# Kernel tuning notes

Measured on AMD Instinct MI355X. Metric: run time of the kernel, lower is better.

Reference implementation:

```python
import jax, jax.numpy as jnp
import numpy as np

N_NODES = 50000
N_EDGES = 800000
D_IN = 16


def gcn_conv(x, edge_index, W, b, n_nodes):
    """PyG GCNConv: x' = D^{-1/2} (A + I) D^{-1/2} X W + b (add_self_loops=True)."""
    h = x @ W  # [N, d_out] - transform before propagate (small d => cheaper)
    src = jnp.concatenate([edge_index[0], jnp.arange(n_nodes)])  # add self-loops
    dst = jnp.concatenate([edge_index[1], jnp.arange(n_nodes)])
    deg = jax.ops.segment_sum(jnp.ones_like(dst, dtype=h.dtype), dst,
                              num_segments=n_nodes)  # in-degree incl. self-loop
    deg_inv_sqrt = jnp.where(deg > 0, jax.lax.rsqrt(deg), 0.0)
    norm = deg_inv_sqrt[src] * deg_inv_sqrt[dst]  # [E+N]
    msg = h[src] * norm[:, None]                  # gather + scale
    out = jax.ops.segment_sum(msg, dst, num_segments=n_nodes)  # scatter-add
    return out + b


def setup_inputs() -> dict:
    key = jax.random.key(0)
    ks = jax.random.split(key, 16)
    d = D_IN
    x = jax.random.normal(ks[0], (N_NODES, d), dtype=jnp.float32)
    edge_index = jax.random.randint(ks[1], (2, N_EDGES), 0, N_NODES, dtype=jnp.int64)

    def glorot(k, fan_in, fan_out):
        s = (6.0 / (fan_in + fan_out)) ** 0.5
        return jax.random.uniform(k, (fan_in, fan_out), jnp.float32, -s, s)

    return {
        "x": x,
        "edge_index": edge_index,
        "W1": glorot(ks[2], d, 2 * d),      "b1": jnp.zeros((2 * d,), jnp.float32),
        "W2": glorot(ks[3], 2 * d, 4 * d),  "b2": jnp.zeros((4 * d,), jnp.float32),
        "W3": glorot(ks[4], 4 * d, 8 * d),  "b3": jnp.zeros((8 * d,), jnp.float32),
        "Wl1": glorot(ks[5], 8 * d, 4 * d), "bl1": jnp.zeros((4 * d,), jnp.float32),
        "Wl2": glorot(ks[6], 4 * d, 2 * d), "bl2": jnp.zeros((2 * d,), jnp.float32),
        "Wl3": glorot(ks[7], 2 * d, d),     "bl3": jnp.zeros((d,), jnp.float32),
    }


def reference(x, edge_index, W1, b1, W2, b2, W3, b3, Wl1, bl1, Wl2, bl2, Wl3, bl3):
    n = x.shape[0]
    # note: original applies relu twice per conv; relu is idempotent
    out = jax.nn.relu(gcn_conv(x, edge_index, W1, b1, n))
    out = jax.nn.relu(gcn_conv(out, edge_index, W2, b2, n))
    out = jax.nn.relu(gcn_conv(out, edge_index, W3, b3, n))
    out = jax.nn.relu(out @ Wl1 + bl1)
    out = jax.nn.relu(out @ Wl2 + bl2)
    out = jax.nn.relu(out @ Wl3 + bl3)
    return out
```

## Files before the change

kernel.cpp:

```cpp
#include <hip/hip_runtime.h>

#define TPB 256
#define TE  2048
#define MAXB 6144

typedef _Float16 half_t;
typedef _Float16 half4 __attribute__((ext_vector_type(4)));
typedef _Float16 half8 __attribute__((ext_vector_type(8)));
typedef float float8v __attribute__((ext_vector_type(8)));

static inline int cdiv(int a, int b) { return (a + b - 1) / b; }


__global__ void k_zero_int(int* p, int n) {
    int i = blockIdx.x * blockDim.x + threadIdx.x;
    if (i < n) p[i] = 0;
}

__global__ void k_bhist(const int* __restrict__ dst, int* __restrict__ gcnt,
                        int e, int nb) {
    __shared__ int lc[256];
    for (int t = threadIdx.x; t < nb; t += TPB) lc[t] = 0;
    __syncthreads();
    for (int i = blockIdx.x * TPB + threadIdx.x; i < e; i += gridDim.x * TPB)
        atomicAdd(&lc[dst[i] >> 8], 1);
    __syncthreads();
    for (int t = threadIdx.x; t < nb; t += TPB) {
        int v = lc[t];
        if (v) atomicAdd(&gcnt[t], v);
    }
}

__global__ void k_bscan(const int* __restrict__ gcnt, int* __restrict__ bstart,
                        int* __restrict__ bcur, int nb, int e) {
    __shared__ int s[256];
    int t = threadIdx.x;
    int v = (t < nb) ? gcnt[t] : 0;
    s[t] = v;
    __syncthreads();
    for (int d = 1; d < 256; d <<= 1) {
        int x = (t >= d) ? s[t - d] : 0;
        __syncthreads();
        s[t] += x;
        __syncthreads();
    }
    if (t < nb) { int ex = s[t] - v; bstart[t] = ex; bcur[t] = ex; }
    if (t == 0) bstart[nb] = e;
}

__global__ void __launch_bounds__(TPB)
k_binscatter(const int* __restrict__ src, const int* __restrict__ dst,
             int* __restrict__ bcur, unsigned int* __restrict__ gbuf,
             int e, int nb) {
    __shared__ int lcnt[256], loffs[256], lcur[256], gres[256];
    __shared__ int ss[256];
    __shared__ unsigned int ldata[TE];
    const int base = blockIdx.x * TE;
    const int cnt = min(TE, e - base);
    for (int t = threadIdx.x; t < nb; t += TPB) lcnt[t] = 0;
    __syncthreads();

    unsigned int myv[TE / TPB];
    int myb[TE / TPB];
#pragma unroll
    for (int k = 0; k < TE / TPB; ++k) {
        int j = threadIdx.x + k * TPB;
        if (j < cnt) {
            int d = dst[base + j], s = src[base + j];
            int b = d >> 8;
            myv[k] = ((unsigned)b << 24) | ((unsigned)(d & 255) << 16) | (unsigned)s;
            myb[k] = b;
            atomicAdd(&lcnt[b], 1);
        } else myb[k] = -1;
    }
    __syncthreads();
    {
        int t = threadIdx.x;
        int v = (t < nb) ? lcnt[t] : 0;
        ss[t] = v;
        __syncthreads();
        for (int d = 1; d < 256; d <<= 1) {
            int x = (t >= d) ? ss[t - d] : 0;
            __syncthreads();
            ss[t] += x;
            __syncthreads();
        }
        if (t < nb) { loffs[t] = ss[t] - v; lcur[t] = ss[t] - v; }
    }
    __syncthreads();
    for (int t = threadIdx.x; t < nb; t += TPB)
        if (lcnt[t]) gres[t] = atomicAdd(&bcur[t], lcnt[t]);
#pragma unroll
    for (int k = 0; k < TE / TPB; ++k) {
        if (myb[k] >= 0) {
            int p = atomicAdd(&lcur[myb[k]], 1);
            ldata[p] = myv[k];
        }
    }
    __syncthreads();
    for (int j = threadIdx.x; j < cnt; j += TPB) {
        unsigned int v = ldata[j];
        int b = v >> 24;
        gbuf[gres[b] + (j - loffs[b])] = v & 0xFFFFFFu;
    }
}

__global__ void __launch_bounds__(TPB)
k_csr(const unsigned int* __restrict__ gbuf, const int* __restrict__ bstart,
      int* __restrict__ offs, float* __restrict__ dinv, int* __restrict__ ssrc,
      int n, int e) {
    __shared__ int cnt[256], loffs2[256], lcur2[256], ss[256];
    __shared__ int stage[MAXB];
    const int b = blockIdx.x;
    const int s0 = bstart[b], s1 = bstart[b + 1];
    const int m = s1 - s0;
    cnt[threadIdx.x] = 0;
    __syncthreads();
    for (int j = threadIdx.x; j < m; j += TPB)
        atomicAdd(&cnt[(gbuf[s0 + j] >> 16) & 255], 1);
    __syncthreads();
    {
        int t = threadIdx.x;
        int v = cnt[t];
        ss[t] = v;
        __syncthreads();
        for (int d = 1; d < 256; d <<= 1) {
            int x = (t >= d) ? ss[t - d] : 0;
            __syncthreads();
            ss[t] += x;
            __syncthreads();
        }
        loffs2[t] = ss[t] - v;
        lcur2[t] = ss[t] - v;
        int node = b * 256 + t;
        if (node < n) {
            offs[node] = s0 + loffs2[t];
            dinv[node] = rsqrtf((float)v + 1.0f);
        }
    }
    __syncthreads();
    for (int j = threadIdx.x; j < m; j += TPB) {
        unsigned int v = gbuf[s0 + j];
        int p = atomicAdd(&lcur2[(v >> 16) & 255], 1);
        stage[p] = (int)(v & 0xFFFFu);
    }
    __syncthreads();
    for (int j = threadIdx.x; j < m; j += TPB) ssrc[s0 + j] = stage[j];
    if (b == 0 && threadIdx.x == 0) offs[n] = e;
}


__global__ void k_scale(const float* __restrict__ x, const float* __restrict__ dinv,
                        half_t* __restrict__ G, int n) {
    int idx = blockIdx.x * blockDim.x + threadIdx.x;
    if (idx >= n * 2) return;
    float d = dinv[idx >> 1];
    float8v v = ((const float8v*)x)[idx];
    half8 h;
#pragma unroll
    for (int q = 0; q < 8; ++q) h[q] = (half_t)(v[q] * d);
    ((half8*)G)[idx] = h;
}

template<int DI, int DO, int R, bool SCALE, bool OUT_HALF, bool WHALF>
__global__ void __launch_bounds__(TPB, 4)
k_conv(const int* __restrict__ offs, const int* __restrict__ ssrc,
       const half_t* __restrict__ G, const float* __restrict__ dinv,
       const float* __restrict__ W, const float* __restrict__ b,
       void* __restrict__ outp, int n) {
    constexpr int CT = DO / 4;
    constexpr int RT = TPB / CT;
    constexpr int TM = RT * R;
    constexpr int K4 = DI / 4;
    constexpr int PX = K4 + 1;
    constexpr int C  = DI / 8;
    static_assert(TM * C == TPB, "gather/gemm tile mismatch");
    __shared__ float4 sW4[WHALF ? 1 : DI * CT];
    __shared__ half4  sWh[WHALF ? DI * CT : 1];
    __shared__ float4 sX4[TM * PX];
    const int tid = threadIdx.x;
    const int r0 = blockIdx.x * TM;

    const float4* Wg = (const float4*)W;
    for (int t = tid; t < DI * CT; t += TPB) {
        float4 w = Wg[t];
        if (WHALF) {
            half4 h;
            h.x = (half_t)w.x; h.y = (half_t)w.y;
            h.z = (half_t)w.z; h.w = (half_t)w.w;
            sWh[t] = h;
        } else {
            sW4[t] = w;
        }
    }

    {
        int gr = tid / C;
        int gc = tid - gr * C;
        int row = r0 + gr;
        float8v acc;
#pragma unroll
        for (int q = 0; q < 8; ++q) acc[q] = 0.f;
        if (row < n) {
            const half8* Grow = (const half8*)G;
            half8 hs = Grow[(size_t)row * C + gc];
#pragma unroll
            for (int q = 0; q < 8; ++q) acc[q] = (float)hs[q];
            int s0 = offs[row], s1 = offs[row + 1];
            int j = s0;
            for (; j + 3 < s1; j += 4) {
                int sa = ssrc[j], sb = ssrc[j + 1];
                int sc = ssrc[j + 2], sd = ssrc[j + 3];
                half8 ga = Grow[(size_t)sa * C + gc];
                half8 gb = Grow[(size_t)sb * C + gc];
                half8 gch = Grow[(size_t)sc * C + gc];
                half8 gd = Grow[(size_t)sd * C + gc];
#pragma unroll
                for (int q = 0; q < 8; ++q)
                    acc[q] += ((float)ga[q] + (float)gb[q]) + ((float)gch[q] + (float)gd[q]);
            }
            for (; j < s1; ++j) {
                half8 ga = Grow[(size_t)ssrc[j] * C + gc];
#pragma unroll
                for (int q = 0; q < 8; ++q) acc[q] += (float)ga[q];
            }
            float di = dinv[row];
#pragma unroll
            for (int q = 0; q < 8; ++q) acc[q] *= di;
        }
        sX4[gr * PX + 2 * gc]     = make_float4(acc[0], acc[1], acc[2], acc[3]);
        sX4[gr * PX + 2 * gc + 1] = make_float4(acc[4], acc[5], acc[6], acc[7]);
    }
    __syncthreads();

    const int c = tid & (CT - 1);
    const int rg = tid / CT;
    const int rbase = rg * R;
    float4 acc[R];
#pragma unroll
    for (int r = 0; r < R; ++r) acc[r] = make_float4(0.f, 0.f, 0.f, 0.f);

#pragma unroll 2
    for (int k4 = 0; k4 < K4; ++k4) {
        float4 xv[R];
#pragma unroll
        for (int r = 0; r < R; ++r) xv[r] = sX4[(rbase + r) * PX + k4];
#pragma unroll
        for (int kk = 0; kk < 4; ++kk) {
            float4 wv;
            if (WHALF) {
                half4 wh = sWh[(k4 * 4 + kk) * CT + c];
                wv = make_float4((float)wh.x, (float)wh.y, (float)wh.z, (float)wh.w);
            } else {
                wv = sW4[(k4 * 4 + kk) * CT + c];
            }
#pragma unroll
            for (int r = 0; r < R; ++r) {
                float xs = (kk == 0) ? xv[r].x : (kk == 1) ? xv[r].y
                         : (kk == 2) ? xv[r].z : xv[r].w;
                acc[r].x += xs * wv.x; acc[r].y += xs * wv.y;
                acc[r].z += xs * wv.z; acc[r].w += xs * wv.w;
            }
        }
    }

    float4 bc = ((const float4*)b)[c];
#pragma unroll
    for (int r = 0; r < R; ++r) {
        int row = r0 + rbase + r;
        if (row < n) {
            float4 o;
            o.x = fmaxf(acc[r].x + bc.x, 0.f);
            o.y = fmaxf(acc[r].y + bc.y, 0.f);
            o.z = fmaxf(acc[r].z + bc.z, 0.f);
            o.w = fmaxf(acc[r].w + bc.w, 0.f);
            if (SCALE) {
                float d = dinv[row];
                o.x *= d; o.y *= d; o.z *= d; o.w *= d;
            }
            if (OUT_HALF) {
                half4 h;
                h.x = (half_t)o.x; h.y = (half_t)o.y;
                h.z = (half_t)o.z; h.w = (half_t)o.w;
                ((half4*)outp)[(size_t)row * CT + c] = h;
            } else {
                ((float4*)outp)[(size_t)row * CT + c] = o;
            }
        }
    }
}

__global__ void __launch_bounds__(256, 2)
k_head(const half_t* __restrict__ X,
       const float* __restrict__ W1, const float* __restrict__ b1,
       const float* __restrict__ W2, const float* __restrict__ b2,
       const float* __restrict__ W3, const float* __restrict__ b3,
       float* __restrict__ out, int n) {
    __shared__ half_t hW1[128 * 64];
    __shared__ half_t hW2[64 * 32];
    __shared__ half_t hW3[32 * 16];
    __shared__ float h1[64 * 65];
    __shared__ float h2[64 * 33];
    const int tid = threadIdx.x;
    const int r0 = blockIdx.x * 64;

    for (int t = tid; t < 128 * 64; t += 256) hW1[t] = (half_t)W1[t];
    for (int t = tid; t < 64 * 32; t += 256) hW2[t] = (half_t)W2[t];
    for (int t = tid; t < 32 * 16; t += 256) hW3[t] = (half_t)W3[t];
    __syncthreads();

    {
        const int c4 = tid & 15;
        const int rowg = tid >> 4;
        const half8* Xr = (const half8*)X;
        float acc[4][4];
#pragma unroll
        for (int r = 0; r < 4; ++r)
#pragma unroll
            for (int j = 0; j < 4; ++j) acc[r][j] = 0.f;
        for (int k8 = 0; k8 < 16; ++k8) {
            half8 xh[4];
#pragma unroll
            for (int r = 0; r < 4; ++r) {
                int row = r0 + rowg * 4 + r;
                if (row < n) xh[r] = Xr[(size_t)row * 16 + k8];
                else { half8 z; for (int q = 0; q < 8; ++q) z[q] = (half_t)0.f; xh[r] = z; }
            }
#pragma unroll
            for (int q = 0; q < 8; ++q) {
                int k = k8 * 8 + q;
                half4 w = *(const half4*)&hW1[k * 64 + c4 * 4];
                float w0 = (float)w.x, w1 = (float)w.y, w2 = (float)w.z, w3 = (float)w.w;
#pragma unroll
                for (int r = 0; r < 4; ++r) {
                    float xs = (float)xh[r][q];
                    acc[r][0] += xs * w0; acc[r][1] += xs * w1;
                    acc[r][2] += xs * w2; acc[r][3] += xs * w3;
                }
            }
        }
        float4 bc = ((const float4*)b1)[c4];
#pragma unroll
        for (int r = 0; r < 4; ++r) {
            int rl = rowg * 4 + r;
            h1[rl * 65 + c4 * 4 + 0] = fmaxf(acc[r][0] + bc.x, 0.f);
            h1[rl * 65 + c4 * 4 + 1] = fmaxf(acc[r][1] + bc.y, 0.f);
            h1[rl * 65 + c4 * 4 + 2] = fmaxf(acc[r][2] + bc.z, 0.f);
            h1[rl * 65 + c4 * 4 + 3] = fmaxf(acc[r][3] + bc.w, 0.f);
        }
    }
    __syncthreads();

    {
        const int c4 = tid & 7;
        const int rowg = tid >> 3;
        float acc[2][4];
#pragma unroll
        for (int r = 0; r < 2; ++r)
#pragma unroll
            for (int j = 0; j < 4; ++j) acc[r][j] = 0.f;
#pragma unroll 4
        for (int k = 0; k < 64; ++k) {
            half4 w = *(const half4*)&hW2[k * 32 + c4 * 4];
            float w0 = (float)w.x, w1 = (float)w.y, w2 = (float)w.z, w3 = (float)w.w;
#pragma unroll
            for (int r = 0; r < 2; ++r) {
                float xs = h1[(rowg * 2 + r) * 65 + k];
                acc[r][0] += xs * w0; acc[r][1] += xs * w1;
                acc[r][2] += xs * w2; acc[r][3] += xs * w3;
            }
        }
        float4 bc = ((const float4*)b2)[c4];
#pragma unroll
        for (int r = 0; r < 2; ++r) {
            int rl = rowg * 2 + r;
            h2[rl * 33 + c4 * 4 + 0] = fmaxf(acc[r][0] + bc.x, 0.f);
            h2[rl * 33 + c4 * 4 + 1] = fmaxf(acc[r][1] + bc.y, 0.f);
            h2[rl * 33 + c4 * 4 + 2] = fmaxf(acc[r][2] + bc.z, 0.f);
            h2[rl * 33 + c4 * 4 + 3] = fmaxf(acc[r][3] + bc.w, 0.f);
        }
    }
    __syncthreads();

    {
        const int c4 = tid & 3;
        const int rl = tid >> 2;
        float a0 = 0.f, a1 = 0.f, a2 = 0.f, a3 = 0.f;
#pragma unroll 4
        for (int k = 0; k < 32; ++k) {
            half4 w = *(const half4*)&hW3[k * 16 + c4 * 4];
            float xs = h2[rl * 33 + k];
            a0 += xs * (float)w.x; a1 += xs * (float)w.y;
            a2 += xs * (float)w.z; a3 += xs * (float)w.w;
        }
        int row = r0 + rl;
        if (row < n) {
            float4 bc = ((const float4*)b3)[c4];
            float4 o;
            o.x = fmaxf(a0 + bc.x, 0.f);
            o.y = fmaxf(a1 + bc.y, 0.f);
            o.z = fmaxf(a2 + bc.z, 0.f);
            o.w = fmaxf(a3 + bc.w, 0.f);
            ((float4*)out)[(size_t)row * 4 + c4] = o;
        }
    }
}

extern "C" void kernel_launch(void* const* d_in, const int* in_sizes, int n_in,
                              void* d_out, int out_size, void* d_ws, size_t ws_size,
                              hipStream_t stream) {
    const float* x   = (const float*)d_in[0];
    const int*   ei  = (const int*)d_in[1];
    const float* W1  = (const float*)d_in[2];
    const float* bb1 = (const float*)d_in[3];
    const float* W2  = (const float*)d_in[4];
    const float* bb2 = (const float*)d_in[5];
    const float* W3  = (const float*)d_in[6];
    const float* bb3 = (const float*)d_in[7];
    const float* Wl1 = (const float*)d_in[8];
    const float* bl1 = (const float*)d_in[9];
    const float* Wl2 = (const float*)d_in[10];
    const float* bl2 = (const float*)d_in[11];
    const float* Wl3 = (const float*)d_in[12];
    const float* bl3 = (const float*)d_in[13];
    float* out = (float*)d_out;

    const int n = in_sizes[0] / 16;
    const int e = in_sizes[1] / 2;
    const int* src = ei;
    const int* dst = ei + e;
    const int nb = cdiv(n, 256);

    char* p = (char*)d_ws;
    auto alloc = [&](size_t bytes) {
        char* r = p;
        p += (bytes + 255) & ~(size_t)255;
        return r;
    };
    float*        dinv   = (float*)        alloc((size_t)n * 4);
    int*          offs   = (int*)          alloc((size_t)(n + 1) * 4);
    int*          gcnt   = (int*)          alloc(256 * 4);
    int*          bstart = (int*)          alloc(257 * 4);
    int*          bcur   = (int*)          alloc(256 * 4);
    unsigned int* gbuf   = (unsigned int*) alloc((size_t)e * 4);
    int*          ssrc   = (int*)          alloc((size_t)e * 4);
    half_t*       H1     = (half_t*)       alloc((size_t)n * 64 * 2);
    half_t*       H2     = (half_t*)       alloc((size_t)n * 32 * 2);
    half_t*       X3h    = (half_t*)       alloc((size_t)n * 128 * 2);

    k_zero_int<<<1, 256, 0, stream>>>(gcnt, nb);
    k_bhist<<<512, TPB, 0, stream>>>(dst, gcnt, e, nb);
    k_bscan<<<1, 256, 0, stream>>>(gcnt, bstart, bcur, nb, e);
    k_binscatter<<<cdiv(e, TE), TPB, 0, stream>>>(src, dst, bcur, gbuf, e, nb);
    k_csr<<<nb, TPB, 0, stream>>>(gbuf, bstart, offs, dinv, ssrc, n, e);

    k_scale<<<cdiv(n * 2, TPB), TPB, 0, stream>>>(x, dinv, H1, n);
    k_conv<16, 32, 4, true, true, false><<<cdiv(n, 128), TPB, 0, stream>>>(
        offs, ssrc, H1, dinv, W1, bb1, H2, n);
    k_conv<32, 64, 4, true, true, false><<<cdiv(n, 64), TPB, 0, stream>>>(
        offs, ssrc, H2, dinv, W2, bb2, H1, n);
    k_conv<64, 128, 4, false, true, true><<<cdiv(n, 32), TPB, 0, stream>>>(
        offs, ssrc, H1, dinv, W3, bb3, X3h, n);

    k_head<<<cdiv(n, 64), 256, 0, stream>>>(X3h, Wl1, bl1, Wl2, bl2, Wl3, bl3, out, n);
}
```

Before: 219.6 us.

## Fuse scan and scale into CSR build, shrink source indices, degree-sort conv rows

Removes the standalone bucket-scan kernel by recomputing the prefix scan redundantly in each binscatter and CSR block. The bcur2 cursors start at zero (zeroed alongside gcnt) and are added to the per-block scan result. The x scaling is folded into the CSR kernel, and source indices are stored as 16-bit values to halve index traffic. Each conv block sorts its rows by degree so lanes with similar edge counts run together, which adds a small rank computation and extra syncs per block. The 16-bit indices rely on node ids fitting in 16 bits (N=50000).

```diff
diff --git a/kernel.cpp b/kernel.cpp
--- a/kernel.cpp
+++ b/kernel.cpp
@@ -31,40 +31,37 @@
     }
 }
 
-__global__ void k_bscan(const int* __restrict__ gcnt, int* __restrict__ bstart,
-                        int* __restrict__ bcur, int nb, int e) {
-    __shared__ int s[256];
-    int t = threadIdx.x;
-    int v = (t < nb) ? gcnt[t] : 0;
-    s[t] = v;
-    __syncthreads();
-    for (int d = 1; d < 256; d <<= 1) {
-        int x = (t >= d) ? s[t - d] : 0;
-        __syncthreads();
-        s[t] += x;
-        __syncthreads();
-    }
-    if (t < nb) { int ex = s[t] - v; bstart[t] = ex; bcur[t] = ex; }
-    if (t == 0) bstart[nb] = e;
-}
-
 __global__ void __launch_bounds__(TPB)
 k_binscatter(const int* __restrict__ src, const int* __restrict__ dst,
-             int* __restrict__ bcur, unsigned int* __restrict__ gbuf,
-             int e, int nb) {
+             const int* __restrict__ gcnt, int* __restrict__ bcur2,
+             unsigned int* __restrict__ gbuf, int e, int nb) {
     __shared__ int lcnt[256], loffs[256], lcur[256], gres[256];
     __shared__ int ss[256];
     __shared__ unsigned int ldata[TE];
+    const int tid = threadIdx.x;
     const int base = blockIdx.x * TE;
     const int cnt = min(TE, e - base);
-    for (int t = threadIdx.x; t < nb; t += TPB) lcnt[t] = 0;
+
+    {
+        int v = (tid < nb) ? gcnt[tid] : 0;
+        ss[tid] = v;
+        __syncthreads();
+        for (int d = 1; d < 256; d <<= 1) {
+            int x2 = (tid >= d) ? ss[tid - d] : 0;
+            __syncthreads();
+            ss[tid] += x2;
+            __syncthreads();
+        }
+        gres[tid] = ss[tid] - v;
+        lcnt[tid] = 0;
+    }
     __syncthreads();
 
     unsigned int myv[TE / TPB];
     int myb[TE / TPB];
 #pragma unroll
     for (int k = 0; k < TE / TPB; ++k) {
-        int j = threadIdx.x + k * TPB;
+        int j = tid + k * TPB;
         if (j < cnt) {
             int d = dst[base + j], s = src[base + j];
             int b = d >> 8;
@@ -75,21 +72,19 @@
     }
     __syncthreads();
     {
-        int t = threadIdx.x;
-        int v = (t < nb) ? lcnt[t] : 0;
-        ss[t] = v;
+        int v = (tid < nb) ? lcnt[tid] : 0;
+        ss[tid] = v;
         __syncthreads();
         for (int d = 1; d < 256; d <<= 1) {
-            int x = (t >= d) ? ss[t - d] : 0;
-            __syncthreads();
-            ss[t] += x;
-            __syncthreads();
-        }
-        if (t < nb) { loffs[t] = ss[t] - v; lcur[t] = ss[t] - v; }
-    }
-    __syncthreads();
-    for (int t = threadIdx.x; t < nb; t += TPB)
-        if (lcnt[t]) gres[t] = atomicAdd(&bcur[t], lcnt[t]);
+            int x2 = (tid >= d) ? ss[tid - d] : 0;
+            __syncthreads();
+            ss[tid] += x2;
+            __syncthreads();
+        }
+        if (tid < nb) { loffs[tid] = ss[tid] - v; lcur[tid] = ss[tid] - v; }
+    }
+    __syncthreads();
+    if (tid < nb && lcnt[tid]) gres[tid] += atomicAdd(&bcur2[tid], lcnt[tid]);
 #pragma unroll
     for (int k = 0; k < TE / TPB; ++k) {
         if (myb[k] >= 0) {
@@ -98,7 +93,7 @@
         }
     }
     __syncthreads();
-    for (int j = threadIdx.x; j < cnt; j += TPB) {
+    for (int j = tid; j < cnt; j += TPB) {
         unsigned int v = ldata[j];
         int b = v >> 24;
         gbuf[gres[b] + (j - loffs[b])] = v & 0xFFFFFFu;
@@ -106,65 +101,84 @@
 }
 
 __global__ void __launch_bounds__(TPB)
-k_csr(const unsigned int* __restrict__ gbuf, const int* __restrict__ bstart,
-      int* __restrict__ offs, float* __restrict__ dinv, int* __restrict__ ssrc,
-      int n, int e) {
-    __shared__ int cnt[256], loffs2[256], lcur2[256], ss[256];
-    __shared__ int stage[MAXB];
+k_csr(const unsigned int* __restrict__ gbuf, const int* __restrict__ gcnt,
+      const float* __restrict__ x, int* __restrict__ offs,
+      float* __restrict__ dinv, unsigned short* __restrict__ ssrc,
+      half_t* __restrict__ G, int n, int e, int nb) {
+    __shared__ int ss[256], cnt[256], loffs2[256], lcur2[256];
+    __shared__ float sdinv[256];
+    __shared__ unsigned short stage[MAXB];
     const int b = blockIdx.x;
-    const int s0 = bstart[b], s1 = bstart[b + 1];
+    const int t = threadIdx.x;
+
+    {
+        int v = (t < nb) ? gcnt[t] : 0;
+        ss[t] = v;
+        __syncthreads();
+        for (int d = 1; d < 256; d <<= 1) {
+            int x2 = (t >= d) ? ss[t - d] : 0;
+            __syncthreads();
+            ss[t] += x2;
+            __syncthreads();
+        }
+    }
+    const int s0 = (b > 0) ? ss[b - 1] : 0;
+    const int s1 = ss[b];
     const int m = s1 - s0;
-    cnt[threadIdx.x] = 0;
-    __syncthreads();
-    for (int j = threadIdx.x; j < m; j += TPB)
+    __syncthreads();
+    cnt[t] = 0;
+    __syncthreads();
+    for (int j = t; j < m; j += TPB)
         atomicAdd(&cnt[(gbuf[s0 + j] >> 16) & 255], 1);
     __syncthreads();
     {
-        int t = threadIdx.x;
         int v = cnt[t];
         ss[t] = v;
         __syncthreads();
         for (int d = 1; d < 256; d <<= 1) {
-            int x = (t >= d) ? ss[t - d] : 0;
-            __syncthreads();
-            ss[t] += x;
+            int x2 = (t >= d) ? ss[t - d] : 0;
+            __syncthreads();
+            ss[t] += x2;
             __syncthreads();
         }
         loffs2[t] = ss[t] - v;
         lcur2[t] = ss[t] - v;
+        float di = rsqrtf((float)v + 1.0f);
+        sdinv[t] = di;
         int node = b * 256 + t;
         if (node < n) {
             offs[node] = s0 + loffs2[t];
-            dinv[node] = rsqrtf((float)v + 1.0f);
-        }
-    }
-    __syncthreads();
-    for (int j = threadIdx.x; j < m; j += TPB) {
+            dinv[node] = di;
+        }
+    }
+    __syncthreads();
+    for (int j = t; j < m; j += TPB) {
         unsigned int v = gbuf[s0 + j];
         int p = atomicAdd(&lcur2[(v >> 16) & 255], 1);
-        stage[p] = (int)(v & 0xFFFFu);
-    }
-    __syncthreads();
-    for (int j = threadIdx.x; j < m; j += TPB) ssrc[s0 + j] = stage[j];
-    if (b == 0 && threadIdx.x == 0) offs[n] = e;
-}
-
-
-__global__ void k_scale(const float* __restrict__ x, const float* __restrict__ dinv,
-                        half_t* __restrict__ G, int n) {
-    int idx = blockIdx.x * blockDim.x + threadIdx.x;
-    if (idx >= n * 2) return;
-    float d = dinv[idx >> 1];
-    float8v v = ((const float8v*)x)[idx];
-    half8 h;
-#pragma unroll
-    for (int q = 0; q < 8; ++q) h[q] = (half_t)(v[q] * d);
-    ((half8*)G)[idx] = h;
+        stage[p] = (unsigned short)(v & 0xFFFFu);
+    }
+    __syncthreads();
+    for (int j = t; j < m; j += TPB) ssrc[s0 + j] = stage[j];
+    if (b == 0 && t == 0) offs[n] = e;
+
+    const int base = b * 256;
+    const int cn = min(256, n - base);
+    const float4* X4 = (const float4*)x;
+    half4* G4 = (half4*)G;
+    for (int j = t; j < cn * 4; j += TPB) {
+        int nl = j >> 2, k4 = j & 3;
+        float4 v = X4[(size_t)(base + nl) * 4 + k4];
+        float d = sdinv[nl];
+        half4 h;
+        h.x = (half_t)(v.x * d); h.y = (half_t)(v.y * d);
+        h.z = (half_t)(v.z * d); h.w = (half_t)(v.w * d);
+        G4[(size_t)(base + nl) * 4 + k4] = h;
+    }
 }
 
 template<int DI, int DO, int R, bool SCALE, bool OUT_HALF, bool WHALF>
 __global__ void __launch_bounds__(TPB, 4)
-k_conv(const int* __restrict__ offs, const int* __restrict__ ssrc,
+k_conv(const int* __restrict__ offs, const unsigned short* __restrict__ ssrc,
        const half_t* __restrict__ G, const float* __restrict__ dinv,
        const float* __restrict__ W, const float* __restrict__ b,
        void* __restrict__ outp, int n) {
@@ -178,6 +192,8 @@
     __shared__ float4 sW4[WHALF ? 1 : DI * CT];
     __shared__ half4  sWh[WHALF ? DI * CT : 1];
     __shared__ float4 sX4[TM * PX];
+    __shared__ int soffs[TM + 1];
+    __shared__ unsigned char perm[TM];
     const int tid = threadIdx.x;
     const int r0 = blockIdx.x * TM;
 
@@ -193,11 +209,24 @@
             sW4[t] = w;
         }
     }
-
-    {
-        int gr = tid / C;
-        int gc = tid - gr * C;
-        int row = r0 + gr;
+    if (tid <= TM) soffs[tid] = offs[min(r0 + tid, n)];
+    __syncthreads();
+    if (tid < TM) {
+        int d = soffs[tid + 1] - soffs[tid];
+        int rank = 0;
+        for (int j = 0; j < TM; ++j) {
+            int dj = soffs[j + 1] - soffs[j];
+            rank += (dj > d) || (dj == d && j < tid);
+        }
+        perm[rank] = (unsigned char)tid;
+    }
+    __syncthreads();
+
+    {
+        int slot = tid / C;
+        int gc = tid - slot * C;
+        int lrow = perm[slot];
+        int row = r0 + lrow;
         float8v acc;
 #pragma unroll
         for (int q = 0; q < 8; ++q) acc[q] = 0.f;
@@ -206,7 +235,7 @@
             half8 hs = Grow[(size_t)row * C + gc];
 #pragma unroll
             for (int q = 0; q < 8; ++q) acc[q] = (float)hs[q];
-            int s0 = offs[row], s1 = offs[row + 1];
+            int s0 = soffs[lrow], s1 = soffs[lrow + 1];
             int j = s0;
             for (; j + 3 < s1; j += 4) {
                 int sa = ssrc[j], sb = ssrc[j + 1];
@@ -228,8 +257,8 @@
 #pragma unroll
             for (int q = 0; q < 8; ++q) acc[q] *= di;
         }
-        sX4[gr * PX + 2 * gc]     = make_float4(acc[0], acc[1], acc[2], acc[3]);
-        sX4[gr * PX + 2 * gc + 1] = make_float4(acc[4], acc[5], acc[6], acc[7]);
+        sX4[lrow * PX + 2 * gc]     = make_float4(acc[0], acc[1], acc[2], acc[3]);
+        sX4[lrow * PX + 2 * gc + 1] = make_float4(acc[4], acc[5], acc[6], acc[7]);
     }
     __syncthreads();
 
@@ -437,24 +466,21 @@
         p += (bytes + 255) & ~(size_t)255;
         return r;
     };
-    float*        dinv   = (float*)        alloc((size_t)n * 4);
-    int*          offs   = (int*)          alloc((size_t)(n + 1) * 4);
-    int*          gcnt   = (int*)          alloc(256 * 4);
-    int*          bstart = (int*)          alloc(257 * 4);
-    int*          bcur   = (int*)          alloc(256 * 4);
-    unsigned int* gbuf   = (unsigned int*) alloc((size_t)e * 4);
-    int*          ssrc   = (int*)          alloc((size_t)e * 4);
-    half_t*       H1     = (half_t*)       alloc((size_t)n * 64 * 2);
-    half_t*       H2     = (half_t*)       alloc((size_t)n * 32 * 2);
-    half_t*       X3h    = (half_t*)       alloc((size_t)n * 128 * 2);
-
-    k_zero_int<<<1, 256, 0, stream>>>(gcnt, nb);
+    float*          dinv   = (float*)         alloc((size_t)n * 4);
+    int*            offs   = (int*)           alloc((size_t)(n + 1) * 4);
+    int*            gcnt   = (int*)           alloc(256 * 4);
+    int*            bcur2  = (int*)           alloc(256 * 4);
+    unsigned int*   gbuf   = (unsigned int*)  alloc((size_t)e * 4);
+    unsigned short* ssrc   = (unsigned short*)alloc((size_t)e * 2);
+    half_t*         H1     = (half_t*)        alloc((size_t)n * 64 * 2);
+    half_t*         H2     = (half_t*)        alloc((size_t)n * 32 * 2);
+    half_t*         X3h    = (half_t*)        alloc((size_t)n * 128 * 2);
+
+    k_zero_int<<<2, 256, 0, stream>>>(gcnt, 512);
     k_bhist<<<512, TPB, 0, stream>>>(dst, gcnt, e, nb);
-    k_bscan<<<1, 256, 0, stream>>>(gcnt, bstart, bcur, nb, e);
-    k_binscatter<<<cdiv(e, TE), TPB, 0, stream>>>(src, dst, bcur, gbuf, e, nb);
-    k_csr<<<nb, TPB, 0, stream>>>(gbuf, bstart, offs, dinv, ssrc, n, e);
-
-    k_scale<<<cdiv(n * 2, TPB), TPB, 0, stream>>>(x, dinv, H1, n);
+    k_binscatter<<<cdiv(e, TE), TPB, 0, stream>>>(src, dst, gcnt, bcur2, gbuf, e, nb);
+    k_csr<<<nb, TPB, 0, stream>>>(gbuf, gcnt, x, offs, dinv, ssrc, H1, n, e, nb);
+
     k_conv<16, 32, 4, true, true, false><<<cdiv(n, 128), TPB, 0, stream>>>(
         offs, ssrc, H1, dinv, W1, bb1, H2, n);
     k_conv<32, 64, 4, true, true, false><<<cdiv(n, 64), TPB, 0, stream>>>(
```

New measurement: 222.0 us. No clear change (+1.1%).
